# Kernel optimization log

Hardware: AMD Instinct MI355X
Metric: run time of the kernel (lower is better)

## Reference

```python
import jax, jax.numpy as jnp
import numpy as np

B, D, H, W = 32, 64, 64, 64
K = 1024

def setup_inputs() -> dict:
    key = jax.random.key(0)
    k1, k2 = jax.random.split(key)
    x = jax.random.normal(k1, (B, D, H, W), dtype=jnp.float32)
    # nn.Parameter(torch.rand(embeddings_dim, num_embeddings)) -> uniform [0,1)
    emb = jax.random.uniform(k2, (D, K), dtype=jnp.float32)
    return {"x": x, "emb": emb}


def reference(x, emb):
    # x: [B, D, H, W], emb: [D, K]
    b, d, h, w = x.shape
    xf = jnp.transpose(x, (0, 2, 3, 1)).reshape(-1, d)  # [N, D], N = B*H*W
    # squared L2 distance (same argmin as torch.norm(.,2) distance)
    d2 = (
        jnp.sum(xf * xf, axis=-1, keepdims=True)
        - 2.0 * (xf @ emb)
        + jnp.sum(emb * emb, axis=0)
    )  # [N, K]
    argmin = jnp.argmin(d2, axis=-1)  # [N]
    # gather codebook vectors: emb.T[argmin] -> [N, D]
    q = jnp.take(emb.T, argmin, axis=0)
    result = jnp.transpose(q.reshape(b, h, w, d), (0, 3, 1, 2))  # [B, D, H, W]
    return result, argmin.reshape(b, h, w)
```

## Files before the change

kernel.cpp:

```cpp
#include <hip/hip_runtime.h>


using half8  = __attribute__((ext_vector_type(8))) _Float16;
using half4  = __attribute__((ext_vector_type(4))) _Float16;
using f32x16 = __attribute__((ext_vector_type(16))) float;

#define XPITCH 72

__global__ void prep_kernel(const float* __restrict__ emb,
                            float* __restrict__ e2,
                            _Float16* __restrict__ eTh,
                            _Float16* __restrict__ eTl) {
    int k = blockIdx.x * 64 + threadIdx.x;
    float s = 0.f;
#pragma unroll
    for (int c = 0; c < 8; ++c) {
        half8 hv, lv;
#pragma unroll
        for (int j = 0; j < 8; ++j) {
            float v = emb[(c * 8 + j) * 1024 + k];
            s = fmaf(v, v, s);
            _Float16 h = (_Float16)v;
            hv[j] = h;
            lv[j] = (_Float16)(v - (float)h);
        }
        *(half8*)(eTh + k * 64 + c * 8) = hv;
        *(half8*)(eTl + k * 64 + c * 8) = lv;
    }
    e2[k] = s;
}

__launch_bounds__(256, 2)
__global__ void vq_kernel(const float* __restrict__ x,
                          const _Float16* __restrict__ eTh,
                          const _Float16* __restrict__ eTl,
                          const float* __restrict__ e2,
                          const float* __restrict__ emb,
                          float* __restrict__ outq,
                          float* __restrict__ outidx) {
    __shared__ _Float16 sxh[128 * XPITCH];
    __shared__ _Float16 sxl[128 * XPITCH];
    __shared__ __align__(16) _Float16 sB[2][4096];
    __shared__ int samin[128];

    const int tx = threadIdx.x;
    const int n0 = blockIdx.x * 128;
    const int bb = n0 >> 12;
    const int hw = n0 & 4095;
    const float* xbase = x + bb * 262144 + hw;

    {
        const int p     = tx & 127;
        const int dbase = (tx >> 7) << 5;
#pragma unroll
        for (int it = 0; it < 8; ++it) {
            int d0 = dbase + it * 4;
            float v0 = xbase[(d0 + 0) * 4096 + p];
            float v1 = xbase[(d0 + 1) * 4096 + p];
            float v2 = xbase[(d0 + 2) * 4096 + p];
            float v3 = xbase[(d0 + 3) * 4096 + p];
            _Float16 h0 = (_Float16)v0, h1 = (_Float16)v1,
                     h2 = (_Float16)v2, h3 = (_Float16)v3;
            half4 hv = {h0, h1, h2, h3};
            half4 lv = {(_Float16)(v0 - (float)h0), (_Float16)(v1 - (float)h1),
                        (_Float16)(v2 - (float)h2), (_Float16)(v3 - (float)h3)};
            *(half4*)(sxh + p * XPITCH + d0) = hv;
            *(half4*)(sxl + p * XPITCH + d0) = lv;
        }
    }
    __syncthreads();

    const int lane = tx & 63;
    const int w    = tx >> 6;
    const int c    = lane & 31;
    const int hi   = lane >> 5;
    const int pxb  = w << 5;

    half8 ah[4], al[4];
#pragma unroll
    for (int ch = 0; ch < 4; ++ch) {
        ah[ch] = *(const half8*)(sxh + (pxb + c) * XPITCH + ch * 16 + hi * 8);
        al[ch] = *(const half8*)(sxl + (pxb + c) * XPITCH + ch * 16 + hi * 8);
    }
    asm volatile("" ::: "memory");

    int Dofs[4];
#pragma unroll
    for (int ch = 0; ch < 4; ++ch) {
        const int y = c * 128 + ch * 32 + hi * 16;
        Dofs[ch] = y ^ ((c & 7) << 4);
    }

    const int Lb = tx * 16;
    const int Sb = Lb ^ (((Lb >> 7) & 7) << 4);
    const char* gH = (const char*)eTh + Sb;
    const char* gL = (const char*)eTl + Sb;

#define STAGE(BUF, TT)                                                        \
    {                                                                         \
        __builtin_amdgcn_global_load_lds(                                     \
            (const __attribute__((address_space(1))) unsigned int*)(gH + ((TT) << 12)), \
            (__attribute__((address_space(3))) unsigned int*)(sB[BUF] + (w << 9)),       \
            16, 0, 0);                                                        \
        __builtin_amdgcn_global_load_lds(                                     \
            (const __attribute__((address_space(1))) unsigned int*)(gL + ((TT) << 12)), \
            (__attribute__((address_space(3))) unsigned int*)(sB[BUF] + 2048 + (w << 9)),\
            16, 0, 0);                                                        \
    }

    float best[16];
    int   bestt[16];
#pragma unroll
    for (int i = 0; i < 16; ++i) { best[i] = 3.4e38f; bestt[i] = 0; }

    STAGE(0, 0);
    __syncthreads();

#pragma unroll 1
    for (int t = 0; t < 32; ++t) {
        const int cur = t & 1;
        if (t < 31) STAGE(cur ^ 1, t + 1);

        const float e2v = e2[(t << 5) + c];
        const char* bbase = (const char*)sB[cur];
        half8 bh_[4], bl_[4];
#pragma unroll
        for (int ch = 0; ch < 4; ++ch) {
            bh_[ch] = *(const half8*)(bbase + Dofs[ch]);
            bl_[ch] = *(const half8*)(bbase + 4096 + Dofs[ch]);
        }

        f32x16 a1 = {};
        f32x16 a2 = {};
#pragma unroll
        for (int ch = 0; ch < 4; ++ch)
            a1 = __builtin_amdgcn_mfma_f32_32x32x16_f16(al[ch], bl_[ch], a1, 0, 0, 0);
#pragma unroll
        for (int ch = 0; ch < 4; ++ch)
            a1 = __builtin_amdgcn_mfma_f32_32x32x16_f16(al[ch], bh_[ch], a1, 0, 0, 0);
#pragma unroll
        for (int ch = 0; ch < 4; ++ch)
            a2 = __builtin_amdgcn_mfma_f32_32x32x16_f16(ah[ch], bl_[ch], a2, 0, 0, 0);
#pragma unroll
        for (int ch = 0; ch < 4; ++ch)
            a2 = __builtin_amdgcn_mfma_f32_32x32x16_f16(ah[ch], bh_[ch], a2, 0, 0, 0);

#pragma unroll
        for (int r = 0; r < 16; ++r) {
            float dist = fmaf(-2.f, a1[r] + a2[r], e2v);
            if (dist < best[r]) { best[r] = dist; bestt[r] = t; }
        }
        __syncthreads();
    }

#pragma unroll
    for (int r = 0; r < 16; ++r) {
        float bv = best[r];
        int   bk = (bestt[r] << 5) + c;
#pragma unroll
        for (int m = 1; m < 32; m <<= 1) {
            float ov = __shfl_xor(bv, m, 64);
            int   ok = __shfl_xor(bk, m, 64);
            if (ov < bv || (ov == bv && ok < bk)) { bv = ov; bk = ok; }
        }
        if (c == 0) {
            const int row = (r & 3) + 8 * (r >> 2) + 4 * hi;
            samin[pxb + row] = bk;
        }
    }
    __syncthreads();

    if (tx < 128) outidx[n0 + tx] = (float)samin[tx];

    const int p = tx & 127;
    const int drow = tx >> 7;
    const int amin = samin[p];
    float* obase = outq + bb * 262144 + hw + p;
#pragma unroll
    for (int it = 0; it < 32; ++it) {
        int d = (it << 1) + drow;
        obase[d * 4096] = emb[d * 1024 + amin];
    }
}

extern "C" void kernel_launch(void* const* d_in, const int* in_sizes, int n_in,
                              void* d_out, int out_size, void* d_ws, size_t ws_size,
                              hipStream_t stream) {
    const float* x   = (const float*)d_in[0];
    const float* emb = (const float*)d_in[1];
    float* outq   = (float*)d_out;
    float* outidx = outq + 8388608;

    float*    e2  = (float*)d_ws;
    _Float16* eTh = (_Float16*)((char*)d_ws + 4096);
    _Float16* eTl = (_Float16*)((char*)d_ws + 4096 + 131072);

    prep_kernel<<<16, 64, 0, stream>>>(emb, e2, eTh, eTl);
    vq_kernel<<<1024, 256, 0, stream>>>(x, eTh, eTl, e2, emb, outq, outidx);
}
```

Baseline: 178.7 us.

## Load x fragments directly to registers, drop LDS staging, merge accumulators

Removes the shared-memory staging of the x tile (hi/lo fp16 split) and instead has each lane load its MFMA A-fragment straight from global memory and split it in registers. It also merges the two MFMA accumulators into one and raises the launch-bounds occupancy hint from 2 to 4 blocks per CU. The goal is to cut LDS footprint, one barrier and register pressure so more blocks stay resident to hide latency. The cost is strided, less coalesced global reads of x and a single serial MFMA dependency chain of 16 ops per tile, which reduces instruction-level parallelism.

```diff
diff --git a/kernel.cpp b/kernel.cpp
--- a/kernel.cpp
+++ b/kernel.cpp
@@ -2,10 +2,7 @@
 
 
 using half8  = __attribute__((ext_vector_type(8))) _Float16;
-using half4  = __attribute__((ext_vector_type(4))) _Float16;
 using f32x16 = __attribute__((ext_vector_type(16))) float;
-
-#define XPITCH 72
 
 __global__ void prep_kernel(const float* __restrict__ emb,
                             float* __restrict__ e2,
@@ -30,7 +27,7 @@
     e2[k] = s;
 }
 
-__launch_bounds__(256, 2)
+__launch_bounds__(256, 4)
 __global__ void vq_kernel(const float* __restrict__ x,
                           const _Float16* __restrict__ eTh,
                           const _Float16* __restrict__ eTl,
@@ -38,8 +35,6 @@
                           const float* __restrict__ emb,
                           float* __restrict__ outq,
                           float* __restrict__ outidx) {
-    __shared__ _Float16 sxh[128 * XPITCH];
-    __shared__ _Float16 sxl[128 * XPITCH];
     __shared__ __align__(16) _Float16 sB[2][4096];
     __shared__ int samin[128];
 
@@ -48,27 +43,6 @@
     const int bb = n0 >> 12;
     const int hw = n0 & 4095;
     const float* xbase = x + bb * 262144 + hw;
-
-    {
-        const int p     = tx & 127;
-        const int dbase = (tx >> 7) << 5;
-#pragma unroll
-        for (int it = 0; it < 8; ++it) {
-            int d0 = dbase + it * 4;
-            float v0 = xbase[(d0 + 0) * 4096 + p];
-            float v1 = xbase[(d0 + 1) * 4096 + p];
-            float v2 = xbase[(d0 + 2) * 4096 + p];
-            float v3 = xbase[(d0 + 3) * 4096 + p];
-            _Float16 h0 = (_Float16)v0, h1 = (_Float16)v1,
-                     h2 = (_Float16)v2, h3 = (_Float16)v3;
-            half4 hv = {h0, h1, h2, h3};
-            half4 lv = {(_Float16)(v0 - (float)h0), (_Float16)(v1 - (float)h1),
-                        (_Float16)(v2 - (float)h2), (_Float16)(v3 - (float)h3)};
-            *(half4*)(sxh + p * XPITCH + d0) = hv;
-            *(half4*)(sxl + p * XPITCH + d0) = lv;
-        }
-    }
-    __syncthreads();
 
     const int lane = tx & 63;
     const int w    = tx >> 6;
@@ -79,8 +53,13 @@
     half8 ah[4], al[4];
 #pragma unroll
     for (int ch = 0; ch < 4; ++ch) {
-        ah[ch] = *(const half8*)(sxh + (pxb + c) * XPITCH + ch * 16 + hi * 8);
-        al[ch] = *(const half8*)(sxl + (pxb + c) * XPITCH + ch * 16 + hi * 8);
+#pragma unroll
+        for (int j = 0; j < 8; ++j) {
+            float v = xbase[(ch * 16 + hi * 8 + j) * 4096 + pxb + c];
+            _Float16 h = (_Float16)v;
+            ah[ch][j] = h;
+            al[ch][j] = (_Float16)(v - (float)h);
+        }
     }
     asm volatile("" ::: "memory");
 
@@ -130,24 +109,23 @@
             bl_[ch] = *(const half8*)(bbase + 4096 + Dofs[ch]);
         }
 
-        f32x16 a1 = {};
-        f32x16 a2 = {};
+        f32x16 a = {};
 #pragma unroll
         for (int ch = 0; ch < 4; ++ch)
-            a1 = __builtin_amdgcn_mfma_f32_32x32x16_f16(al[ch], bl_[ch], a1, 0, 0, 0);
+            a = __builtin_amdgcn_mfma_f32_32x32x16_f16(al[ch], bl_[ch], a, 0, 0, 0);
 #pragma unroll
         for (int ch = 0; ch < 4; ++ch)
-            a1 = __builtin_amdgcn_mfma_f32_32x32x16_f16(al[ch], bh_[ch], a1, 0, 0, 0);
+            a = __builtin_amdgcn_mfma_f32_32x32x16_f16(al[ch], bh_[ch], a, 0, 0, 0);
 #pragma unroll
         for (int ch = 0; ch < 4; ++ch)
-            a2 = __builtin_amdgcn_mfma_f32_32x32x16_f16(ah[ch], bl_[ch], a2, 0, 0, 0);
+            a = __builtin_amdgcn_mfma_f32_32x32x16_f16(ah[ch], bl_[ch], a, 0, 0, 0);
 #pragma unroll
         for (int ch = 0; ch < 4; ++ch)
-            a2 = __builtin_amdgcn_mfma_f32_32x32x16_f16(ah[ch], bh_[ch], a2, 0, 0, 0);
+            a = __builtin_amdgcn_mfma_f32_32x32x16_f16(ah[ch], bh_[ch], a, 0, 0, 0);
 
 #pragma unroll
         for (int r = 0; r < 16; ++r) {
-            float dist = fmaf(-2.f, a1[r] + a2[r], e2v);
+            float dist = fmaf(-2.f, a[r], e2v);
             if (dist < best[r]) { best[r] = dist; bestt[r] = t; }
         }
         __syncthreads();
```

Measured after the change: 158.1 us. -11.6%, faster.
